# Optimization experiments

Hardware: AMD Instinct MI355X
Metric: run time of the kernel (lower is better)

## Reference

```python
import jax, jax.numpy as jnp
import numpy as np

NUM_HEADS = 12

def setup_inputs() -> dict:
    key = jax.random.key(0)
    ks = jax.random.split(key, 9)
    B, N, C = 4, 1024, 768
    hd = C // NUM_HEADS  # 64
    return {
        "x": jax.random.normal(ks[0], (B, N, C), dtype=jnp.float32),
        "prev_attn": jax.random.uniform(ks[1], (B, NUM_HEADS, N, N), dtype=jnp.float32) / N,
        "qkv_w": jax.random.normal(ks[2], (3 * C, C), dtype=jnp.float32) * 0.02,
        "proj_w": jax.random.normal(ks[3], (C, C), dtype=jnp.float32) * 0.02,
        "proj_b": jax.random.normal(ks[4], (C,), dtype=jnp.float32) * 0.02,
        "bp_w1": jax.random.normal(ks[5], (hd // 2, 2 * hd), dtype=jnp.float32) * 0.02,
        "bp_b1": jax.random.normal(ks[6], (hd // 2,), dtype=jnp.float32) * 0.02,
        "bp_w2": jax.random.normal(ks[7], (3, hd // 2), dtype=jnp.float32) * 0.02,
        "bp_b2": jax.random.normal(ks[8], (3,), dtype=jnp.float32) * 0.02,
    }

def reference(x, prev_attn, qkv_w, proj_w, proj_b, bp_w1, bp_b1, bp_w2, bp_b2):
    B, N, C = x.shape
    H = NUM_HEADS
    hd = C // H
    scale = hd ** -0.5
    # qkv projection: [B,N,3C] -> [3,B,H,N,hd]
    qkv = (x @ qkv_w.T).reshape(B, N, 3, H, hd).transpose(2, 0, 3, 1, 4)
    q, k, v = qkv[0], qkv[1], qkv[2]
    # scaled dot-product scores [B,H,N,N]
    attn_logits = jnp.einsum('bhnd,bhmd->bhnm', q, k) * scale
    cur_attn = jax.nn.softmax(attn_logits, axis=-1)
    # per-(b,h,n) bias MLP on concat(q,k): [B,H,N,2*hd] -> [B,H,N,3]
    qk = jnp.concatenate((q, k), axis=-1)
    h1 = jax.nn.relu(jnp.einsum('bhnd,od->bhno', qk, bp_w1) + bp_b1)
    bias = jnp.abs(jnp.einsum('bhno,po->bhnp', h1, bp_w2) + bp_b2)  # [B,H,N,3]
    # blend current attention, previous attention, and uniform term
    attn = (cur_attn * (1.0 + bias[..., 0:1])
            + prev_attn * bias[..., 1:2]
            - bias[..., 2:3] / N)
    out = jnp.einsum('bhnm,bhmd->bhnd', attn, v)  # [B,H,N,hd]
    out = out.transpose(0, 2, 1, 3).reshape(B, N, C)
    out = out @ proj_w.T + proj_b
    return (out, cur_attn)
```

## Files before the change

kernel.cpp:

```cpp
#include <hip/hip_runtime.h>

typedef __bf16 bf16_t;
typedef __bf16 bf16x8 __attribute__((ext_vector_type(8)));
typedef __bf16 bf16x4 __attribute__((ext_vector_type(4)));
typedef float f32x4 __attribute__((ext_vector_type(4)));

static constexpr int Bb = 4, Hh = 12, Nn = 1024, Cc = 768, HD = 64;
static constexpr int OUT0 = Bb * Nn * Cc;

#define GLD16(gp, lp)                                                       \
  __builtin_amdgcn_global_load_lds(                                         \
      (const __attribute__((address_space(1))) unsigned int*)(gp),          \
      (__attribute__((address_space(3))) unsigned int*)(lp), 16, 0, 0)

__global__ __launch_bounds__(256) void convert_all(
    const float* __restrict__ x, const float* __restrict__ qw, const float* __restrict__ pw,
    bf16_t* __restrict__ xb, bf16_t* __restrict__ qwb, bf16_t* __restrict__ pwb) {
  const int NX = (Bb * Nn * Cc) / 4;
  const int NQ = (3 * Cc * Cc) / 4;
  int i = blockIdx.x * 256 + threadIdx.x;
  const float4* src;
  bf16_t* dst;
  int off;
  if (i < NX) { src = (const float4*)x; dst = xb; off = i; }
  else if (i < NX + NQ) { src = (const float4*)qw; dst = qwb; off = i - NX; }
  else { src = (const float4*)pw; dst = pwb; off = i - NX - NQ; }
  float4 v = src[off];
  bf16x4 o;
  o[0] = (bf16_t)v.x; o[1] = (bf16_t)v.y; o[2] = (bf16_t)v.z; o[3] = (bf16_t)v.w;
  *(bf16x4*)(dst + (size_t)off * 4) = o;
}

__global__ __launch_bounds__(256) void gemm_qkv(
    const bf16_t* __restrict__ A, const bf16_t* __restrict__ Bm,
    bf16_t* __restrict__ q_bf, bf16_t* __restrict__ k_bf, bf16_t* __restrict__ vT_bf) {
  __shared__ bf16_t As[128 * 32];
  __shared__ bf16_t Bs[128 * 32];
  const int tid = threadIdx.x;
  const int lane = tid & 63;
  const int w = tid >> 6;
  const int wr = w >> 1, wc = w & 1;
  const int g = lane >> 4, r = lane & 15;
  const int m0 = (blockIdx.x / 18) << 7;
  const int n0 = (blockIdx.x % 18) << 7;

  const f32x4 fz = {0.f, 0.f, 0.f, 0.f};
  f32x4 acc[4][4];
#pragma unroll
  for (int i = 0; i < 4; i++)
#pragma unroll
    for (int j = 0; j < 4; j++) acc[i][j] = fz;

  for (int k0 = 0; k0 < 768; k0 += 32) {
#pragma unroll
    for (int c = 0; c < 2; c++) {
      int row = w * 32 + c * 16 + (lane >> 2);
      int kof = (lane & 3) << 3;
      GLD16(&A[(size_t)(m0 + row) * 768 + k0 + kof], (char*)As + w * 2048 + c * 1024);
      GLD16(&Bm[(size_t)(n0 + row) * 768 + k0 + kof], (char*)Bs + w * 2048 + c * 1024);
    }
    __syncthreads();
    bf16x8 af[4], bfv[4];
#pragma unroll
    for (int i = 0; i < 4; i++) af[i] = *(const bf16x8*)&As[(wr * 64 + i * 16 + r) * 32 + g * 8];
#pragma unroll
    for (int j = 0; j < 4; j++) bfv[j] = *(const bf16x8*)&Bs[(wc * 64 + j * 16 + r) * 32 + g * 8];
#pragma unroll
    for (int i = 0; i < 4; i++)
#pragma unroll
      for (int j = 0; j < 4; j++)
        acc[i][j] = __builtin_amdgcn_mfma_f32_16x16x32_bf16(af[i], bfv[j], acc[i][j], 0, 0, 0);
    __syncthreads();
  }

#pragma unroll
  for (int i = 0; i < 4; i++) {
#pragma unroll
    for (int j = 0; j < 4; j++) {
      int c = n0 + wc * 64 + j * 16 + r;
#pragma unroll
      for (int e = 0; e < 4; e++) {
        int mrow = m0 + wr * 64 + i * 16 + g * 4 + e;
        float val = acc[i][j][e];
        int which = c / 768;
        int cc = c - which * 768;
        int h = cc >> 6, d = cc & 63;
        int b = mrow >> 10, n = mrow & 1023;
        size_t bh = (size_t)(b * Hh + h);
        if (which == 0)      q_bf[(bh * Nn + n) * HD + d] = (bf16_t)val;
        else if (which == 1) k_bf[(bh * Nn + n) * HD + d] = (bf16_t)val;
        else                 vT_bf[(bh * HD + d) * Nn + n] = (bf16_t)val;
      }
    }
  }
}

template <int MODE>
__global__ __launch_bounds__(256) void gemm_bt(
    const bf16_t* __restrict__ A, const bf16_t* __restrict__ Bm, int N, int K,
    float* __restrict__ outF, const float* __restrict__ bias) {
  __shared__ bf16_t As[128 * 40];
  __shared__ bf16_t Bs[128 * 40];
  const int tid = threadIdx.x;
  const int lane = tid & 63;
  const int w = tid >> 6;
  const int wr = w >> 1, wc = w & 1;
  const int g = lane >> 4, r = lane & 15;
  const int ntiles = N >> 7;
  const int m0 = (blockIdx.x / ntiles) << 7;
  const int n0 = (blockIdx.x % ntiles) << 7;

  const f32x4 fz = {0.f, 0.f, 0.f, 0.f};
  f32x4 acc[4][4];
#pragma unroll
  for (int i = 0; i < 4; i++)
#pragma unroll
    for (int j = 0; j < 4; j++) acc[i][j] = fz;

  for (int k0 = 0; k0 < K; k0 += 32) {
#pragma unroll
    for (int p = 0; p < 2; p++) {
      int idx = tid + (p << 8);
      int row = idx >> 2;
      int kof = (idx & 3) << 3;
      *(bf16x8*)&As[row * 40 + kof] = *(const bf16x8*)&A[(size_t)(m0 + row) * K + k0 + kof];
      *(bf16x8*)&Bs[row * 40 + kof] = *(const bf16x8*)&Bm[(size_t)(n0 + row) * K + k0 + kof];
    }
    __syncthreads();
    bf16x8 af[4], bfv[4];
#pragma unroll
    for (int i = 0; i < 4; i++) af[i] = *(const bf16x8*)&As[(wr * 64 + i * 16 + r) * 40 + g * 8];
#pragma unroll
    for (int j = 0; j < 4; j++) bfv[j] = *(const bf16x8*)&Bs[(wc * 64 + j * 16 + r) * 40 + g * 8];
#pragma unroll
    for (int i = 0; i < 4; i++)
#pragma unroll
      for (int j = 0; j < 4; j++)
        acc[i][j] = __builtin_amdgcn_mfma_f32_16x16x32_bf16(af[i], bfv[j], acc[i][j], 0, 0, 0);
    __syncthreads();
  }

#pragma unroll
  for (int i = 0; i < 4; i++) {
#pragma unroll
    for (int j = 0; j < 4; j++) {
      int c = n0 + wc * 64 + j * 16 + r;
#pragma unroll
      for (int e = 0; e < 4; e++) {
        int mrow = m0 + wr * 64 + i * 16 + g * 4 + e;
        outF[(size_t)mrow * N + c] = acc[i][j][e] + bias[c];
      }
    }
  }
}

__global__ __launch_bounds__(256) void bias_mlp(
    const bf16_t* __restrict__ qb, const bf16_t* __restrict__ kb,
    const float* __restrict__ w1, const float* __restrict__ b1,
    const float* __restrict__ w2, const float* __restrict__ b2,
    float* __restrict__ bias4) {
  __shared__ float w1s[32 * 130];
  __shared__ float qks[8][128];
  __shared__ float h1s[8][32];
  const int t = threadIdx.x;
#pragma unroll
  for (int p = 0; p < 16; p++) {
    int idx = p * 256 + t;
    w1s[(idx >> 7) * 130 + (idx & 127)] = w1[idx];
  }
  const int rl = t >> 5, u = t & 31;
  const int rowg = blockIdx.x * 8 + rl;
  {
    int i4 = u * 4;
    const bf16_t* src = (i4 < 64) ? (qb + (size_t)rowg * HD + i4)
                                  : (kb + (size_t)rowg * HD + (i4 - 64));
    bf16x4 vv = *(const bf16x4*)src;
#pragma unroll
    for (int z = 0; z < 4; z++) qks[rl][i4 + z] = (float)vv[z];
  }
  __syncthreads();
  float accv = b1[u];
#pragma unroll 16
  for (int i2 = 0; i2 < 64; i2++) {
    float2 wv = *(const float2*)&w1s[u * 130 + i2 * 2];
    float2 qv = *(const float2*)&qks[rl][i2 * 2];
    accv += wv.x * qv.x + wv.y * qv.y;
  }
  h1s[rl][u] = fmaxf(accv, 0.f);
  __syncthreads();
  if (u < 4) {
    float outv = 0.f;
    if (u < 3) {
      float s = b2[u];
#pragma unroll
      for (int j = 0; j < 32; j++) s += w2[u * 32 + j] * h1s[rl][j];
      float v = fabsf(s);
      outv = (u == 0) ? (1.f + v) : ((u == 1) ? v : -v * (1.f / (float)Nn));
    }
    bias4[(size_t)rowg * 4 + u] = outv;
  }
}

__global__ __launch_bounds__(256, 2) void attn_fused(
    const bf16_t* __restrict__ qb, const bf16_t* __restrict__ kb,
    const bf16_t* __restrict__ vT, const float* __restrict__ prev,
    const float* __restrict__ bias4, float* __restrict__ cur,
    bf16_t* __restrict__ oh) {
  __shared__ char Plb[16 * 2048];
  __shared__ float redmax[16][4];
  __shared__ float redsum[16][4];
  const int bid = blockIdx.x;
  const int tile = (bid & 7) * 384 + (bid >> 3);
  const int bh = tile >> 6, mt = tile & 63;
  const int tid = threadIdx.x;
  const int lane = tid & 63, w = tid >> 6;
  const int g = lane >> 4, r = lane & 15;
  const int row0 = mt << 4;
  const int cbase = w << 8;

  const bf16_t* qp = qb + ((size_t)bh * Nn + row0) * HD;
  const bf16_t* kp = kb + (size_t)bh * Nn * HD;
  bf16x8 qr0 = *(const bf16x8*)&qp[r * HD + g * 8];
  bf16x8 qr1 = *(const bf16x8*)&qp[r * HD + g * 8 + 32];
  bf16x8 qa0, qa1;
#pragma unroll
  for (int j = 0; j < 8; j++) {
    qa0[j] = (bf16_t)((float)qr0[j] * 0.125f);
    qa1[j] = (bf16_t)((float)qr1[j] * 0.125f);
  }
  const f32x4 fz = {0.f, 0.f, 0.f, 0.f};
  f32x4 acc[16];
#pragma unroll
  for (int t = 0; t < 16; t++) {
    int col = cbase + (t << 4) + r;
    bf16x8 kf0 = *(const bf16x8*)&kp[(size_t)col * HD + g * 8];
    bf16x8 kf1 = *(const bf16x8*)&kp[(size_t)col * HD + g * 8 + 32];
    f32x4 z = __builtin_amdgcn_mfma_f32_16x16x32_bf16(kf0, qa0, fz, 0, 0, 0);
    acc[t] = __builtin_amdgcn_mfma_f32_16x16x32_bf16(kf1, qa1, z, 0, 0, 0);
  }

  const float* ppr = prev + (size_t)bh * Nn * Nn + (size_t)(row0 + r) * Nn + cbase + (g << 2);
  float4 pv[16];
#pragma unroll
  for (int t = 0; t < 16; t++) pv[t] = *(const float4*)&ppr[t << 4];
  __builtin_amdgcn_sched_barrier(0);

  float mj = -3.0e38f;
#pragma unroll
  for (int t = 0; t < 16; t++)
#pragma unroll
    for (int e = 0; e < 4; e++) mj = fmaxf(mj, acc[t][e]);
  mj = fmaxf(mj, __shfl_xor(mj, 16, 64));
  mj = fmaxf(mj, __shfl_xor(mj, 32, 64));
  if (lane < 16) redmax[lane][w] = mj;
  __syncthreads();
  float rm;
  {
    float v0 = fmaxf(redmax[r][0], redmax[r][1]);
    rm = fmaxf(v0, fmaxf(redmax[r][2], redmax[r][3]));
  }

  bf16x4 pvb[16];
#pragma unroll
  for (int t = 0; t < 16; t++) {
    pvb[t][0] = (bf16_t)pv[t].x;
    pvb[t][1] = (bf16_t)pv[t].y;
    pvb[t][2] = (bf16_t)pv[t].z;
    pvb[t][3] = (bf16_t)pv[t].w;
  }
  __builtin_amdgcn_sched_barrier(0);

  float sj = 0.f;
  bf16x4 p16[16];
#pragma unroll
  for (int t = 0; t < 16; t++) {
    float e0 = __expf(acc[t][0] - rm);
    float e1 = __expf(acc[t][1] - rm);
    float e2 = __expf(acc[t][2] - rm);
    float e3 = __expf(acc[t][3] - rm);
    sj += (e0 + e1) + (e2 + e3);
    p16[t][0] = (bf16_t)e0;
    p16[t][1] = (bf16_t)e1;
    p16[t][2] = (bf16_t)e2;
    p16[t][3] = (bf16_t)e3;
  }
  sj += __shfl_xor(sj, 16, 64);
  sj += __shfl_xor(sj, 32, 64);
  if (lane < 16) redsum[lane][w] = sj;
  __syncthreads();
  const float inv =
      1.f / (redsum[r][0] + redsum[r][1] + redsum[r][2] + redsum[r][3]);

  const float4 bvr = *(const float4*)&bias4[((size_t)bh * 1024 + row0 + r) * 4];
  const float b0c = bvr.x, b1c = bvr.y, b2c = bvr.z;
  float* cp = cur + (size_t)bh * Nn * Nn + (size_t)(row0 + r) * Nn + cbase + (g << 2);
#pragma unroll
  for (int t = 0; t < 16; t++) {
    float4 p;
    p.x = (float)p16[t][0] * inv;
    p.y = (float)p16[t][1] * inv;
    p.z = (float)p16[t][2] * inv;
    p.w = (float)p16[t][3] * inv;
    *(float4*)&cp[t << 4] = p;
    bf16x4 nb;
    nb[0] = (bf16_t)(b0c * p.x + b1c * (float)pvb[t][0] + b2c);
    nb[1] = (bf16_t)(b0c * p.y + b1c * (float)pvb[t][1] + b2c);
    nb[2] = (bf16_t)(b0c * p.z + b1c * (float)pvb[t][2] + b2c);
    nb[3] = (bf16_t)(b0c * p.w + b1c * (float)pvb[t][3] + b2c);
    int col = cbase + (t << 4) + (g << 2);
    int off = (r * 2048 + col * 2) ^ ((r & 7) << 4);
    *(bf16x4*)(Plb + off) = nb;
  }
  __syncthreads();

  const bf16_t* vrow = vT + (size_t)bh * HD * Nn + (size_t)((w << 4) + r) * Nn;
  f32x4 c0 = fz, c1 = fz, c2 = fz, c3 = fz;
#pragma unroll
  for (int ks = 0; ks < 8; ks++) {
    int kA = ks << 5;
    bf16x8 pA = *(const bf16x8*)(Plb + ((r * 2048 + (kA + g * 8) * 2) ^ ((r & 7) << 4)));
    bf16x8 pB = *(const bf16x8*)(Plb + ((r * 2048 + (256 + kA + g * 8) * 2) ^ ((r & 7) << 4)));
    bf16x8 pC = *(const bf16x8*)(Plb + ((r * 2048 + (512 + kA + g * 8) * 2) ^ ((r & 7) << 4)));
    bf16x8 pD = *(const bf16x8*)(Plb + ((r * 2048 + (768 + kA + g * 8) * 2) ^ ((r & 7) << 4)));
    bf16x8 vA = *(const bf16x8*)&vrow[kA + g * 8];
    bf16x8 vB = *(const bf16x8*)&vrow[256 + kA + g * 8];
    bf16x8 vC = *(const bf16x8*)&vrow[512 + kA + g * 8];
    bf16x8 vD = *(const bf16x8*)&vrow[768 + kA + g * 8];
    c0 = __builtin_amdgcn_mfma_f32_16x16x32_bf16(pA, vA, c0, 0, 0, 0);
    c1 = __builtin_amdgcn_mfma_f32_16x16x32_bf16(pB, vB, c1, 0, 0, 0);
    c2 = __builtin_amdgcn_mfma_f32_16x16x32_bf16(pC, vC, c2, 0, 0, 0);
    c3 = __builtin_amdgcn_mfma_f32_16x16x32_bf16(pD, vD, c3, 0, 0, 0);
  }
  f32x4 osum = (c0 + c1) + (c2 + c3);
  const int b = bh / Hh, h = bh % Hh;
#pragma unroll
  for (int e = 0; e < 4; e++) {
    int nrow = row0 + g * 4 + e;
    oh[((size_t)(b * Nn + nrow)) * Cc + h * HD + (w << 4) + r] = (bf16_t)osum[e];
  }
}

extern "C" void kernel_launch(void* const* d_in, const int* in_sizes, int n_in,
                              void* d_out, int out_size, void* d_ws, size_t ws_size,
                              hipStream_t stream) {
  const float* x      = (const float*)d_in[0];
  const float* prev   = (const float*)d_in[1];
  const float* qkv_w  = (const float*)d_in[2];
  const float* proj_w = (const float*)d_in[3];
  const float* proj_b = (const float*)d_in[4];
  const float* bp_w1  = (const float*)d_in[5];
  const float* bp_b1  = (const float*)d_in[6];
  const float* bp_w2  = (const float*)d_in[7];
  const float* bp_w2b = (const float*)d_in[8];

  float* out0 = (float*)d_out;
  float* cur  = out0 + OUT0;

  char* ws = (char*)d_ws;
  bf16_t* xb    = (bf16_t*)(ws + 0);
  bf16_t* qwb   = (bf16_t*)(ws + 6291456);
  bf16_t* pwb   = (bf16_t*)(ws + 9830400);
  bf16_t* qbf   = (bf16_t*)(ws + 11010048);
  bf16_t* kbf   = (bf16_t*)(ws + 17301504);
  bf16_t* vtb   = (bf16_t*)(ws + 23592960);
  float*  bias4 = (float*)(ws + 29884416);
  bf16_t* ohb   = (bf16_t*)(ws + 30670848);
  if (ws_size < 36962304) return;

  convert_all<<<5376, 256, 0, stream>>>(x, qkv_w, proj_w, xb, qwb, pwb);
  gemm_qkv<<<32 * 18, 256, 0, stream>>>(xb, qwb, qbf, kbf, vtb);
  bias_mlp<<<49152 / 8, 256, 0, stream>>>(qbf, kbf, bp_w1, bp_b1, bp_w2, bp_w2b, bias4);
  attn_fused<<<3072, 256, 0, stream>>>(qbf, kbf, vtb, prev, bias4, cur, ohb);
  gemm_bt<1><<<(4096 / 128) * (768 / 128), 256, 0, stream>>>(
      ohb, pwb, 768, 768, out0, proj_b);
}
```

Before: 248.6 us.

## Stage prev_attn through LDS with async global-to-LDS loads in two halves

```diff
diff --git a/kernel.cpp b/kernel.cpp
--- a/kernel.cpp
+++ b/kernel.cpp
@@ -207,6 +207,7 @@
     const float* __restrict__ bias4, float* __restrict__ cur,
     bf16_t* __restrict__ oh) {
   __shared__ char Plb[16 * 2048];
+  __shared__ char prevLds[4 * 8192];
   __shared__ float redmax[16][4];
   __shared__ float redsum[16][4];
   const int bid = blockIdx.x;
@@ -240,10 +241,9 @@
   }
 
   const float* ppr = prev + (size_t)bh * Nn * Nn + (size_t)(row0 + r) * Nn + cbase + (g << 2);
-  float4 pv[16];
-#pragma unroll
-  for (int t = 0; t < 16; t++) pv[t] = *(const float4*)&ppr[t << 4];
-  __builtin_amdgcn_sched_barrier(0);
+  char* myPrev = prevLds + (w << 13);
+#pragma unroll
+  for (int t = 0; t < 8; t++) GLD16(ppr + (t << 4), myPrev + (t << 10));
 
   float mj = -3.0e38f;
 #pragma unroll
@@ -259,16 +259,6 @@
     float v0 = fmaxf(redmax[r][0], redmax[r][1]);
     rm = fmaxf(v0, fmaxf(redmax[r][2], redmax[r][3]));
   }
-
-  bf16x4 pvb[16];
-#pragma unroll
-  for (int t = 0; t < 16; t++) {
-    pvb[t][0] = (bf16_t)pv[t].x;
-    pvb[t][1] = (bf16_t)pv[t].y;
-    pvb[t][2] = (bf16_t)pv[t].z;
-    pvb[t][3] = (bf16_t)pv[t].w;
-  }
-  __builtin_amdgcn_sched_barrier(0);
 
   float sj = 0.f;
   bf16x4 p16[16];
@@ -294,8 +284,17 @@
   const float4 bvr = *(const float4*)&bias4[((size_t)bh * 1024 + row0 + r) * 4];
   const float b0c = bvr.x, b1c = bvr.y, b2c = bvr.z;
   float* cp = cur + (size_t)bh * Nn * Nn + (size_t)(row0 + r) * Nn + cbase + (g << 2);
-#pragma unroll
-  for (int t = 0; t < 16; t++) {
+
+  f32x4 pv[8];
+#pragma unroll
+  for (int t = 0; t < 8; t++)
+    pv[t] = *(const f32x4*)(myPrev + (t << 10) + (lane << 4));
+  asm volatile("s_waitcnt lgkmcnt(0)" ::: "memory");
+  __builtin_amdgcn_sched_barrier(0);
+#pragma unroll
+  for (int t = 0; t < 8; t++) GLD16(ppr + ((t + 8) << 4), myPrev + (t << 10));
+#pragma unroll
+  for (int t = 0; t < 8; t++) {
     float4 p;
     p.x = (float)p16[t][0] * inv;
     p.y = (float)p16[t][1] * inv;
@@ -303,10 +302,33 @@
     p.w = (float)p16[t][3] * inv;
     *(float4*)&cp[t << 4] = p;
     bf16x4 nb;
-    nb[0] = (bf16_t)(b0c * p.x + b1c * (float)pvb[t][0] + b2c);
-    nb[1] = (bf16_t)(b0c * p.y + b1c * (float)pvb[t][1] + b2c);
-    nb[2] = (bf16_t)(b0c * p.z + b1c * (float)pvb[t][2] + b2c);
-    nb[3] = (bf16_t)(b0c * p.w + b1c * (float)pvb[t][3] + b2c);
+    nb[0] = (bf16_t)(b0c * p.x + b1c * pv[t][0] + b2c);
+    nb[1] = (bf16_t)(b0c * p.y + b1c * pv[t][1] + b2c);
+    nb[2] = (bf16_t)(b0c * p.z + b1c * pv[t][2] + b2c);
+    nb[3] = (bf16_t)(b0c * p.w + b1c * pv[t][3] + b2c);
+    int col = cbase + (t << 4) + (g << 2);
+    int off = (r * 2048 + col * 2) ^ ((r & 7) << 4);
+    *(bf16x4*)(Plb + off) = nb;
+  }
+
+  asm volatile("s_waitcnt vmcnt(0)" ::: "memory");
+  __builtin_amdgcn_sched_barrier(0);
+#pragma unroll
+  for (int t = 0; t < 8; t++)
+    pv[t] = *(const f32x4*)(myPrev + (t << 10) + (lane << 4));
+#pragma unroll
+  for (int t = 8; t < 16; t++) {
+    float4 p;
+    p.x = (float)p16[t][0] * inv;
+    p.y = (float)p16[t][1] * inv;
+    p.z = (float)p16[t][2] * inv;
+    p.w = (float)p16[t][3] * inv;
+    *(float4*)&cp[t << 4] = p;
+    bf16x4 nb;
+    nb[0] = (bf16_t)(b0c * p.x + b1c * pv[t - 8][0] + b2c);
+    nb[1] = (bf16_t)(b0c * p.y + b1c * pv[t - 8][1] + b2c);
+    nb[2] = (bf16_t)(b0c * p.z + b1c * pv[t - 8][2] + b2c);
+    nb[3] = (bf16_t)(b0c * p.w + b1c * pv[t - 8][3] + b2c);
     int col = cbase + (t << 4) + (g << 2);
     int off = (r * 2048 + col * 2) ^ ((r & 7) << 4);
     *(bf16x4*)(Plb + off) = nb;
```

After: 255.3 us. 2.7% more time.
